# Kernel optimization log

Hardware: AMD Instinct MI355X
Metric: run time of the kernel (lower is better)

## Reference

```python
import jax, jax.numpy as jnp
import numpy as np

NV, NE, H, P = 50000, 10000, 256, 400000

def setup_inputs() -> dict:
    key = jax.random.key(0)
    ks = jax.random.split(key, 16)
    s = 1.0 / np.sqrt(H)
    return {
        "v": jax.random.normal(ks[0], (NV, H), jnp.float32),
        "e": jax.random.normal(ks[1], (NE, H), jnp.float32),
        "W_v2e_w": jax.random.normal(ks[2], (H, H), jnp.float32) * s,
        "W_v2e_b": jnp.zeros((H,), jnp.float32),
        "W_e2v_w": jax.random.normal(ks[3], (H, H), jnp.float32) * s,
        "W_e2v_b": jnp.zeros((H,), jnp.float32),
        "n_weight": jax.random.uniform(ks[4], (NV, 1), jnp.float32),
        "e_weight": jax.random.uniform(ks[5], (NE, 1), jnp.float32),
        "n_reg_weight": jax.random.uniform(ks[6], (P, 1), jnp.float32),
        "e_reg_weight": jax.random.uniform(ks[7], (P, 1), jnp.float32),
        "e_reg_sum": jax.random.uniform(ks[8], (NE, 1), jnp.float32) + 1.0,  # positive normalizer
        "n_reg_sum": jax.random.uniform(ks[9], (NV, 1), jnp.float32) + 1.0,
        "pairs_v": jax.random.randint(ks[10], (P,), 0, NV, jnp.int32),  # ve_lists[:,0]
        "eidx": jax.random.randint(ks[11], (P,), 0, NE, jnp.int32),
        "pairs_e": jax.random.randint(ks[12], (P,), 0, NE, jnp.int32),  # ve_lists[:,1]
        "vidx": jax.random.randint(ks[13], (P,), 0, NV, jnp.int32),
    }

def reference(v, e, W_v2e_w, W_v2e_b, W_e2v_w, W_e2v_b, n_weight, e_weight,
              n_reg_weight, e_reg_weight, e_reg_sum, n_reg_sum,
              pairs_v, eidx, pairs_e, vidx):
    # v2e: dense transform on vertices, gather per incidence, scatter-add into edges
    ve = jax.nn.relu(v @ W_v2e_w.T + W_v2e_b)            # [NV,H]
    v_acc = v * n_weight                                 # v *= n_weight * v_fac(=1)
    msg_ve = (ve * n_weight)[pairs_v] * n_reg_weight     # [P,H]
    e_out = e.at[eidx].add(msg_ve) / e_reg_sum           # [NE,H]
    # e2v: dense transform on edges, gather per incidence, scatter-add into vertices
    ev = jax.nn.relu(e_out @ W_e2v_w.T + W_e2v_b)        # [NE,H]
    msg_ev = (ev * e_weight)[pairs_e] * e_reg_weight     # [P,H]
    v_out = v_acc.at[vidx].add(msg_ev) / n_reg_sum       # [NV,H]
    return v_out, e_out
```

## Files before the change

kernel.cpp:

```cpp
#include <hip/hip_runtime.h>
#include <stdint.h>

#define NV 50000
#define NE 10000
#define HD 256
#define NP 400000

#define SE 88
#define SV 36

#define NCH 128
#define CHP (NP / NCH)
#define NW  15000
#define NWE 2500
#define NWV 12500

#define PREP_HBLK NCH
#define PREP_WBLK 16
#define PREP_VBLK 1563

typedef short short8 __attribute__((ext_vector_type(8)));
typedef short short4v __attribute__((ext_vector_type(4)));
typedef float f32x4 __attribute__((ext_vector_type(4)));

__device__ __forceinline__ short f2bf(float f) {
    unsigned int u = __builtin_bit_cast(unsigned int, f);
    u += 0x7FFFu + ((u >> 16) & 1u);
    return (short)(u >> 16);
}
__device__ __forceinline__ float bf2f(short s) {
    unsigned int u = ((unsigned int)(unsigned short)s) << 16;
    return __builtin_bit_cast(float, u);
}

__global__ __launch_bounds__(1024) void prep_kernel(
    const float* __restrict__ v, const float* __restrict__ W1, const float* __restrict__ W2,
    const int* __restrict__ eidx, const int* __restrict__ vidx,
    short* __restrict__ v_bf, short* __restrict__ W_bf,
    int* __restrict__ cnt8,
    int conv_v)
{
    __shared__ int h[NW];
    int b = blockIdx.x;
    int tid = threadIdx.x;
    if (b < PREP_HBLK) {
        for (int w = tid; w < NW; w += 1024) h[w] = 0;
        __syncthreads();
        int base = b * CHP;
        for (int k = tid; k < CHP; k += 1024) {
            int p = base + k;
            int er = eidx[p];
            atomicAdd((unsigned*)&h[er >> 2], 1u << ((er & 3) * 8));
            int rv = 10000 + vidx[p];
            atomicAdd((unsigned*)&h[rv >> 2], 1u << ((rv & 3) * 8));
        }
        __syncthreads();
        for (int w = tid; w < NW; w += 1024) cnt8[b * NW + w] = h[w];
    } else if (b < PREP_HBLK + PREP_WBLK) {
        size_t i = (size_t)(b - PREP_HBLK) * 8192 + (size_t)tid * 8;
        const float* src = (i < 65536) ? (W1 + i) : (W2 + (i - 65536));
        float4 a0 = *(const float4*)src;
        float4 a1 = *(const float4*)(src + 4);
        short8 s;
        s[0] = f2bf(a0.x); s[1] = f2bf(a0.y); s[2] = f2bf(a0.z); s[3] = f2bf(a0.w);
        s[4] = f2bf(a1.x); s[5] = f2bf(a1.y); s[6] = f2bf(a1.z); s[7] = f2bf(a1.w);
        *(short8*)(W_bf + i) = s;
    } else {
        if (!conv_v) return;
        size_t i = (size_t)(b - PREP_HBLK - PREP_WBLK) * 8192 + (size_t)tid * 8;
        if (i >= (size_t)NV * HD) return;
        float4 a0 = *(const float4*)(v + i);
        float4 a1 = *(const float4*)(v + i + 4);
        short8 s;
        s[0] = f2bf(a0.x); s[1] = f2bf(a0.y); s[2] = f2bf(a0.z); s[3] = f2bf(a0.w);
        s[4] = f2bf(a1.x); s[5] = f2bf(a1.y); s[6] = f2bf(a1.z); s[7] = f2bf(a1.w);
        *(short8*)(v_bf + i) = s;
    }
}

__global__ __launch_bounds__(256) void scan_kernel(
    int* __restrict__ cnt8, int* __restrict__ cnt_e, int* __restrict__ cnt_v)
{
    int w = blockIdx.x * 256 + threadIdx.x;
    if (w >= NW) return;
    unsigned acc = 0;
#pragma unroll 8
    for (int c = 0; c < NCH; ++c) {
        unsigned x = (unsigned)cnt8[c * NW + w];
        cnt8[c * NW + w] = (int)acc;
        acc += x;
    }
    int r0 = w * 4;
    int4 t;
    t.x = acc & 0xFF; t.y = (acc >> 8) & 0xFF; t.z = (acc >> 16) & 0xFF; t.w = acc >> 24;
    if (r0 < 10000) *(int4*)&cnt_e[r0] = t;
    else            *(int4*)&cnt_v[r0 - 10000] = t;
}

__global__ __launch_bounds__(1024) void place_kernel(
    const int* __restrict__ eidx, const int* __restrict__ vidx,
    const int* __restrict__ pairs_v, const int* __restrict__ n_reg_w_bits,
    const int* __restrict__ pairs_e, const int* __restrict__ e_reg_w_bits,
    const int* __restrict__ cnt8,
    int2* __restrict__ bkt_e, int2* __restrict__ bkt_v)
{
    __shared__ int h[NWV];
    int b = blockIdx.x;
    int tid = threadIdx.x;
    if (b < NCH) {
        int c = b;
        for (int w = tid; w < NWE; w += 1024) h[w] = cnt8[c * NW + w];
        __syncthreads();
        int base = c * CHP;
        for (int k = tid; k < CHP; k += 1024) {
            int p = base + k;
            int er = eidx[p];
            unsigned old = atomicAdd((unsigned*)&h[er >> 2], 1u << ((er & 3) * 8));
            int s = (old >> ((er & 3) * 8)) & 0xFF;
            if (s < SE) bkt_e[er * SE + s] = make_int2(pairs_v[p], n_reg_w_bits[p]);
        }
    } else {
        int c = b - NCH;
        for (int w = tid; w < NWV; w += 1024) h[w] = cnt8[c * NW + NWE + w];
        __syncthreads();
        int base = c * CHP;
        for (int k = tid; k < CHP; k += 1024) {
            int p = base + k;
            int vr = vidx[p];
            unsigned old = atomicAdd((unsigned*)&h[vr >> 2], 1u << ((vr & 3) * 8));
            int s = (old >> ((vr & 3) * 8)) & 0xFF;
            if (s < SV) bkt_v[vr * SV + s] = make_int2(pairs_e[p], e_reg_w_bits[p]);
        }
    }
}

__global__ __launch_bounds__(256) void gemm_rs(
    const void* __restrict__ Av, int a_bf,
    const short* __restrict__ Wb,
    const float* __restrict__ bias,
    const float* __restrict__ rowscale,
    short* __restrict__ out,
    int M)
{
    __shared__ short As[64 * 256];
    __shared__ short Ws[64 * 256];
    const int tid  = threadIdx.x;
    const int row0 = blockIdx.x * 64;

#pragma unroll
    for (int it = 0; it < 8; ++it) {
        int cl = it * 256 + tid;
        int r  = cl >> 5;
        int c  = cl & 31;
        int gr = row0 + r; gr = gr < M ? gr : M - 1;
        short8 ap;
        if (a_bf) {
            ap = *(const short8*)((const short*)Av + (size_t)gr * HD + (c << 3));
        } else {
            const float* asrc = (const float*)Av + (size_t)gr * HD + (c << 3);
            float4 a0 = *(const float4*)asrc;
            float4 a1 = *(const float4*)(asrc + 4);
            ap[0] = f2bf(a0.x); ap[1] = f2bf(a0.y); ap[2] = f2bf(a0.z); ap[3] = f2bf(a0.w);
            ap[4] = f2bf(a1.x); ap[5] = f2bf(a1.y); ap[6] = f2bf(a1.z); ap[7] = f2bf(a1.w);
        }
        *(short8*)&As[(r << 8) + ((c ^ (r & 7)) << 3)] = ap;
    }

    const int lane = tid & 63;
    const int wv   = tid >> 6;
    const int m16  = lane & 15;
    const int quad = lane >> 4;
    const int arow = (wv << 4) + m16;

    for (int ct = 0; ct < 4; ++ct) {
        __syncthreads();
#pragma unroll
        for (int it = 0; it < 8; ++it) {
            int cl = it * 256 + tid;
            int r  = cl >> 5;
            int c  = cl & 31;
            short8 wp = *(const short8*)(Wb + (size_t)((ct << 6) + r) * HD + (c << 3));
            *(short8*)&Ws[(r << 8) + ((c ^ (r & 7)) << 3)] = wp;
        }
        __syncthreads();

        f32x4 acc[4];
#pragma unroll
        for (int nt = 0; nt < 4; ++nt) acc[nt] = (f32x4){0.f, 0.f, 0.f, 0.f};

#pragma unroll
        for (int ks = 0; ks < 8; ++ks) {
            int c = (ks << 2) + quad;
            short8 afr = *(const short8*)&As[(arow << 8) + ((c ^ (arow & 7)) << 3)];
#pragma unroll
            for (int nt = 0; nt < 4; ++nt) {
                int brow = (nt << 4) + m16;
                short8 bfr = *(const short8*)&Ws[(brow << 8) + ((c ^ (m16 & 7)) << 3)];
                acc[nt] = __builtin_amdgcn_mfma_f32_16x16x32_bf16(afr, bfr, acc[nt], 0, 0, 0);
            }
        }

#pragma unroll
        for (int r = 0; r < 4; ++r) {
            int row = row0 + (wv << 4) + (quad << 2) + r;
            if (row < M) {
                float rs = rowscale[row];
#pragma unroll
                for (int nt = 0; nt < 4; ++nt) {
                    int col = (ct << 6) + (nt << 4) + m16;
                    float val = acc[nt][r] + bias[col];
                    val = fmaxf(val, 0.0f) * rs;
                    out[(size_t)row * HD + col] = f2bf(val);
                }
            }
        }
    }
}

__device__ __forceinline__ void gather_core(
    const short* __restrict__ msg, const int2* __restrict__ bkt,
    int i, int end, int lane, float4& acc)
{
    while (i < end) {
        int n = end - i; n = n < 64 ? n : 64;
        int src = 0; float w = 0.f;
        if (lane < n) {
            int2 m = bkt[i + lane];
            src = m.x;
            w = __builtin_bit_cast(float, m.y);
        }
        int j = 0;
        for (; j + 4 <= n; j += 4) {
            int   s0 = __shfl(src, j),     s1 = __shfl(src, j + 1);
            int   s2 = __shfl(src, j + 2), s3 = __shfl(src, j + 3);
            float w0 = __shfl(w, j),       w1 = __shfl(w, j + 1);
            float w2 = __shfl(w, j + 2),   w3 = __shfl(w, j + 3);
            short4v m0 = *(const short4v*)(msg + ((size_t)s0 << 8) + (lane << 2));
            short4v m1 = *(const short4v*)(msg + ((size_t)s1 << 8) + (lane << 2));
            short4v m2 = *(const short4v*)(msg + ((size_t)s2 << 8) + (lane << 2));
            short4v m3 = *(const short4v*)(msg + ((size_t)s3 << 8) + (lane << 2));
            acc.x += bf2f(m0[0]) * w0; acc.y += bf2f(m0[1]) * w0;
            acc.z += bf2f(m0[2]) * w0; acc.w += bf2f(m0[3]) * w0;
            acc.x += bf2f(m1[0]) * w1; acc.y += bf2f(m1[1]) * w1;
            acc.z += bf2f(m1[2]) * w1; acc.w += bf2f(m1[3]) * w1;
            acc.x += bf2f(m2[0]) * w2; acc.y += bf2f(m2[1]) * w2;
            acc.z += bf2f(m2[2]) * w2; acc.w += bf2f(m2[3]) * w2;
            acc.x += bf2f(m3[0]) * w3; acc.y += bf2f(m3[1]) * w3;
            acc.z += bf2f(m3[2]) * w3; acc.w += bf2f(m3[3]) * w3;
        }
        for (; j < n; ++j) {
            int s0 = __shfl(src, j); float w0 = __shfl(w, j);
            short4v m0 = *(const short4v*)(msg + ((size_t)s0 << 8) + (lane << 2));
            acc.x += bf2f(m0[0]) * w0; acc.y += bf2f(m0[1]) * w0;
            acc.z += bf2f(m0[2]) * w0; acc.w += bf2f(m0[3]) * w0;
        }
        i += n;
    }
}

__global__ __launch_bounds__(256) void gather_e(
    const short* __restrict__ msg,
    const int2* __restrict__ bkt,
    const int* __restrict__ cnt,
    const float* __restrict__ e_in, const float* __restrict__ reg_sum,
    float* __restrict__ out, short* __restrict__ out_bf)
{
    int r    = (blockIdx.x << 2) + (threadIdx.x >> 6);
    int lane = threadIdx.x & 63;
    float4 acc = ((const float4*)(e_in + (size_t)r * HD))[lane];
    int n = cnt[r]; n = n < SE ? n : SE;
    int i0 = r * SE;
    gather_core(msg, bkt, i0, i0 + n, lane, acc);
    float inv = 1.0f / reg_sum[r];
    acc.x *= inv; acc.y *= inv; acc.z *= inv; acc.w *= inv;
    ((float4*)(out + (size_t)r * HD))[lane] = acc;
    if (out_bf) {
        short4v s;
        s[0] = f2bf(acc.x); s[1] = f2bf(acc.y); s[2] = f2bf(acc.z); s[3] = f2bf(acc.w);
        *(short4v*)(out_bf + (size_t)r * HD + (lane << 2)) = s;
    }
}

__global__ __launch_bounds__(256) void gather_v(
    const short* __restrict__ msg,
    const int2* __restrict__ bkt,
    const int* __restrict__ cnt,
    const float* __restrict__ v_f32, const short* __restrict__ v_bf,
    const float* __restrict__ n_w,
    const float* __restrict__ reg_sum, float* __restrict__ out)
{
    int r    = (blockIdx.x << 2) + (threadIdx.x >> 6);
    int lane = threadIdx.x & 63;
    float nw = n_w[r];
    float4 a;
    if (v_bf) {
        short4v b = *(const short4v*)(v_bf + (size_t)r * HD + (lane << 2));
        a.x = bf2f(b[0]); a.y = bf2f(b[1]); a.z = bf2f(b[2]); a.w = bf2f(b[3]);
    } else {
        a = ((const float4*)(v_f32 + (size_t)r * HD))[lane];
    }
    float4 acc; acc.x = a.x * nw; acc.y = a.y * nw; acc.z = a.z * nw; acc.w = a.w * nw;
    int n = cnt[r]; n = n < SV ? n : SV;
    int i0 = r * SV;
    gather_core(msg, bkt, i0, i0 + n, lane, acc);
    float inv = 1.0f / reg_sum[r];
    acc.x *= inv; acc.y *= inv; acc.z *= inv; acc.w *= inv;
    ((float4*)(out + (size_t)r * HD))[lane] = acc;
}

extern "C" void kernel_launch(void* const* d_in, const int* in_sizes, int n_in,
                              void* d_out, int out_size, void* d_ws, size_t ws_size,
                              hipStream_t stream) {
    const float* v   = (const float*)d_in[0];
    const float* e   = (const float*)d_in[1];
    const float* W1  = (const float*)d_in[2];
    const float* b1  = (const float*)d_in[3];
    const float* W2  = (const float*)d_in[4];
    const float* b2  = (const float*)d_in[5];
    const float* n_weight     = (const float*)d_in[6];
    const float* e_weight     = (const float*)d_in[7];
    const float* n_reg_weight = (const float*)d_in[8];
    const float* e_reg_weight = (const float*)d_in[9];
    const float* e_reg_sum    = (const float*)d_in[10];
    const float* n_reg_sum    = (const float*)d_in[11];
    const int* pairs_v = (const int*)d_in[12];
    const int* eidx    = (const int*)d_in[13];
    const int* pairs_e = (const int*)d_in[14];
    const int* vidx    = (const int*)d_in[15];

    float* out      = (float*)d_out;
    float* v_region = out;
    float* e_region = out + (size_t)NV * HD;

    char* ws = (char*)d_ws;
    size_t o = 0;
    short* msg     = (short*)(ws + o); o += (size_t)NV * HD * 2;
    int2*  bkt_e   = (int2*)(ws + o);  o += (size_t)NE * SE * 8;
    int2*  bkt_v   = (int2*)(ws + o);  o += (size_t)NV * SV * 8;
    short* W_bf    = (short*)(ws + o); o += (size_t)2 * 65536 * 2;
    int*   cnt8    = (int*)(ws + o);
    short* e_bf    = (short*)(ws + o); o += (size_t)NCH * NW * 4;
    int*   cnt_e   = (int*)(ws + o);   o += (size_t)NE * 4;
    int*   cnt_v   = (int*)(ws + o);   o += (size_t)NV * 4;
    size_t o_opt = o;
    short* v_bf    = (short*)(ws + o_opt);
    size_t need_full = o_opt + (size_t)NV * HD * 2;
    const int full = (ws_size >= need_full);

    prep_kernel<<<PREP_HBLK + PREP_WBLK + PREP_VBLK, 1024, 0, stream>>>(
        v, W1, W2, eidx, vidx, full ? v_bf : (short*)msg , W_bf,
        cnt8, full);
    scan_kernel<<<(NW + 255) / 256, 256, 0, stream>>>(cnt8, cnt_e, cnt_v);
    place_kernel<<<2 * NCH, 1024, 0, stream>>>(
        eidx, vidx, pairs_v, (const int*)n_reg_weight,
        pairs_e, (const int*)e_reg_weight, cnt8, bkt_e, bkt_v);

    gemm_rs<<<(NV + 63) / 64, 256, 0, stream>>>(
        full ? (const void*)v_bf : (const void*)v, full, W_bf, b1, n_weight, msg, NV);
    gather_e<<<NE / 4, 256, 0, stream>>>(msg, bkt_e, cnt_e,
        e, e_reg_sum, e_region, e_bf);
    gemm_rs<<<(NE + 63) / 64, 256, 0, stream>>>(
        (const void*)e_bf, 1, W_bf + 65536, b2, e_weight, msg, NE);
    gather_v<<<NV / 4, 256, 0, stream>>>(msg, bkt_v, cnt_v,
        v, full ? v_bf : (short*)0, n_weight, n_reg_sum, v_region);
}
```

Measured before the change: 275.1 us.

## Fuse v bf16 conversion into GEMM and restructure gather with preloaded buckets

The standalone fp32-to-bf16 conversion of v in the prep kernel is removed. The first GEMM now reads fp32 v directly, converts it while staging into shared memory, and writes the bf16 copy out for the later gather_v pass, which saves one full read of v. The gather routine is rewritten: each wave loads its bucket window once up front with a single load, the inner loop is unrolled to 8, and two accumulators break the add dependency chain. Bucket buffers are padded by 64 entries so the unconditional 64-lane window load stays in bounds.

```diff
diff --git a/kernel.cpp b/kernel.cpp
--- a/kernel.cpp
+++ b/kernel.cpp
@@ -17,7 +17,6 @@
 
 #define PREP_HBLK NCH
 #define PREP_WBLK 16
-#define PREP_VBLK 1563
 
 typedef short short8 __attribute__((ext_vector_type(8)));
 typedef short short4v __attribute__((ext_vector_type(4)));
@@ -34,11 +33,10 @@
 }
 
 __global__ __launch_bounds__(1024) void prep_kernel(
-    const float* __restrict__ v, const float* __restrict__ W1, const float* __restrict__ W2,
+    const float* __restrict__ W1, const float* __restrict__ W2,
     const int* __restrict__ eidx, const int* __restrict__ vidx,
-    short* __restrict__ v_bf, short* __restrict__ W_bf,
-    int* __restrict__ cnt8,
-    int conv_v)
+    short* __restrict__ W_bf,
+    int* __restrict__ cnt8)
 {
     __shared__ int h[NW];
     int b = blockIdx.x;
@@ -56,7 +54,7 @@
         }
         __syncthreads();
         for (int w = tid; w < NW; w += 1024) cnt8[b * NW + w] = h[w];
-    } else if (b < PREP_HBLK + PREP_WBLK) {
+    } else {
         size_t i = (size_t)(b - PREP_HBLK) * 8192 + (size_t)tid * 8;
         const float* src = (i < 65536) ? (W1 + i) : (W2 + (i - 65536));
         float4 a0 = *(const float4*)src;
@@ -65,16 +63,6 @@
         s[0] = f2bf(a0.x); s[1] = f2bf(a0.y); s[2] = f2bf(a0.z); s[3] = f2bf(a0.w);
         s[4] = f2bf(a1.x); s[5] = f2bf(a1.y); s[6] = f2bf(a1.z); s[7] = f2bf(a1.w);
         *(short8*)(W_bf + i) = s;
-    } else {
-        if (!conv_v) return;
-        size_t i = (size_t)(b - PREP_HBLK - PREP_WBLK) * 8192 + (size_t)tid * 8;
-        if (i >= (size_t)NV * HD) return;
-        float4 a0 = *(const float4*)(v + i);
-        float4 a1 = *(const float4*)(v + i + 4);
-        short8 s;
-        s[0] = f2bf(a0.x); s[1] = f2bf(a0.y); s[2] = f2bf(a0.z); s[3] = f2bf(a0.w);
-        s[4] = f2bf(a1.x); s[5] = f2bf(a1.y); s[6] = f2bf(a1.z); s[7] = f2bf(a1.w);
-        *(short8*)(v_bf + i) = s;
     }
 }
 
@@ -140,6 +128,7 @@
     const float* __restrict__ bias,
     const float* __restrict__ rowscale,
     short* __restrict__ out,
+    short* __restrict__ a_out,
     int M)
 {
     __shared__ short As[64 * 256];
@@ -152,7 +141,8 @@
         int cl = it * 256 + tid;
         int r  = cl >> 5;
         int c  = cl & 31;
-        int gr = row0 + r; gr = gr < M ? gr : M - 1;
+        int gr0 = row0 + r;
+        int gr  = gr0 < M ? gr0 : M - 1;
         short8 ap;
         if (a_bf) {
             ap = *(const short8*)((const short*)Av + (size_t)gr * HD + (c << 3));
@@ -162,6 +152,8 @@
             float4 a1 = *(const float4*)(asrc + 4);
             ap[0] = f2bf(a0.x); ap[1] = f2bf(a0.y); ap[2] = f2bf(a0.z); ap[3] = f2bf(a0.w);
             ap[4] = f2bf(a1.x); ap[5] = f2bf(a1.y); ap[6] = f2bf(a1.z); ap[7] = f2bf(a1.w);
+            if (a_out && gr0 < M)
+                *(short8*)(a_out + (size_t)gr0 * HD + (c << 3)) = ap;
         }
         *(short8*)&As[(r << 8) + ((c ^ (r & 7)) << 3)] = ap;
     }
@@ -217,44 +209,66 @@
     }
 }
 
-__device__ __forceinline__ void gather_core(
-    const short* __restrict__ msg, const int2* __restrict__ bkt,
-    int i, int end, int lane, float4& acc)
-{
-    while (i < end) {
-        int n = end - i; n = n < 64 ? n : 64;
-        int src = 0; float w = 0.f;
-        if (lane < n) {
-            int2 m = bkt[i + lane];
-            src = m.x;
-            w = __builtin_bit_cast(float, m.y);
-        }
-        int j = 0;
-        for (; j + 4 <= n; j += 4) {
-            int   s0 = __shfl(src, j),     s1 = __shfl(src, j + 1);
-            int   s2 = __shfl(src, j + 2), s3 = __shfl(src, j + 3);
-            float w0 = __shfl(w, j),       w1 = __shfl(w, j + 1);
-            float w2 = __shfl(w, j + 2),   w3 = __shfl(w, j + 3);
-            short4v m0 = *(const short4v*)(msg + ((size_t)s0 << 8) + (lane << 2));
-            short4v m1 = *(const short4v*)(msg + ((size_t)s1 << 8) + (lane << 2));
-            short4v m2 = *(const short4v*)(msg + ((size_t)s2 << 8) + (lane << 2));
-            short4v m3 = *(const short4v*)(msg + ((size_t)s3 << 8) + (lane << 2));
-            acc.x += bf2f(m0[0]) * w0; acc.y += bf2f(m0[1]) * w0;
-            acc.z += bf2f(m0[2]) * w0; acc.w += bf2f(m0[3]) * w0;
-            acc.x += bf2f(m1[0]) * w1; acc.y += bf2f(m1[1]) * w1;
-            acc.z += bf2f(m1[2]) * w1; acc.w += bf2f(m1[3]) * w1;
-            acc.x += bf2f(m2[0]) * w2; acc.y += bf2f(m2[1]) * w2;
-            acc.z += bf2f(m2[2]) * w2; acc.w += bf2f(m2[3]) * w2;
-            acc.x += bf2f(m3[0]) * w3; acc.y += bf2f(m3[1]) * w3;
-            acc.z += bf2f(m3[2]) * w3; acc.w += bf2f(m3[3]) * w3;
-        }
-        for (; j < n; ++j) {
-            int s0 = __shfl(src, j); float w0 = __shfl(w, j);
-            short4v m0 = *(const short4v*)(msg + ((size_t)s0 << 8) + (lane << 2));
-            acc.x += bf2f(m0[0]) * w0; acc.y += bf2f(m0[1]) * w0;
-            acc.z += bf2f(m0[2]) * w0; acc.w += bf2f(m0[3]) * w0;
-        }
-        i += n;
+__device__ __forceinline__ void gather_win(
+    const short* __restrict__ msg, int src, int wb, int cnt, int lane,
+    float4& A, float4& B)
+{
+    int j = 0;
+    for (; j + 8 <= cnt; j += 8) {
+        int s0 = __shfl(src, j),     s1 = __shfl(src, j + 1);
+        int s2 = __shfl(src, j + 2), s3 = __shfl(src, j + 3);
+        int s4 = __shfl(src, j + 4), s5 = __shfl(src, j + 5);
+        int s6 = __shfl(src, j + 6), s7 = __shfl(src, j + 7);
+        float w0 = __builtin_bit_cast(float, __shfl(wb, j));
+        float w1 = __builtin_bit_cast(float, __shfl(wb, j + 1));
+        float w2 = __builtin_bit_cast(float, __shfl(wb, j + 2));
+        float w3 = __builtin_bit_cast(float, __shfl(wb, j + 3));
+        float w4 = __builtin_bit_cast(float, __shfl(wb, j + 4));
+        float w5 = __builtin_bit_cast(float, __shfl(wb, j + 5));
+        float w6 = __builtin_bit_cast(float, __shfl(wb, j + 6));
+        float w7 = __builtin_bit_cast(float, __shfl(wb, j + 7));
+        short4v m0 = *(const short4v*)(msg + ((size_t)s0 << 8) + (lane << 2));
+        short4v m1 = *(const short4v*)(msg + ((size_t)s1 << 8) + (lane << 2));
+        short4v m2 = *(const short4v*)(msg + ((size_t)s2 << 8) + (lane << 2));
+        short4v m3 = *(const short4v*)(msg + ((size_t)s3 << 8) + (lane << 2));
+        short4v m4 = *(const short4v*)(msg + ((size_t)s4 << 8) + (lane << 2));
+        short4v m5 = *(const short4v*)(msg + ((size_t)s5 << 8) + (lane << 2));
+        short4v m6 = *(const short4v*)(msg + ((size_t)s6 << 8) + (lane << 2));
+        short4v m7 = *(const short4v*)(msg + ((size_t)s7 << 8) + (lane << 2));
+        A.x += bf2f(m0[0]) * w0; A.y += bf2f(m0[1]) * w0;
+        A.z += bf2f(m0[2]) * w0; A.w += bf2f(m0[3]) * w0;
+        B.x += bf2f(m1[0]) * w1; B.y += bf2f(m1[1]) * w1;
+        B.z += bf2f(m1[2]) * w1; B.w += bf2f(m1[3]) * w1;
+        A.x += bf2f(m2[0]) * w2; A.y += bf2f(m2[1]) * w2;
+        A.z += bf2f(m2[2]) * w2; A.w += bf2f(m2[3]) * w2;
+        B.x += bf2f(m3[0]) * w3; B.y += bf2f(m3[1]) * w3;
+        B.z += bf2f(m3[2]) * w3; B.w += bf2f(m3[3]) * w3;
+        A.x += bf2f(m4[0]) * w4; A.y += bf2f(m4[1]) * w4;
+        A.z += bf2f(m4[2]) * w4; A.w += bf2f(m4[3]) * w4;
+        B.x += bf2f(m5[0]) * w5; B.y += bf2f(m5[1]) * w5;
+        B.z += bf2f(m5[2]) * w5; B.w += bf2f(m5[3]) * w5;
+        A.x += bf2f(m6[0]) * w6; A.y += bf2f(m6[1]) * w6;
+        A.z += bf2f(m6[2]) * w6; A.w += bf2f(m6[3]) * w6;
+        B.x += bf2f(m7[0]) * w7; B.y += bf2f(m7[1]) * w7;
+        B.z += bf2f(m7[2]) * w7; B.w += bf2f(m7[3]) * w7;
+    }
+    for (; j + 2 <= cnt; j += 2) {
+        int s0 = __shfl(src, j), s1 = __shfl(src, j + 1);
+        float w0 = __builtin_bit_cast(float, __shfl(wb, j));
+        float w1 = __builtin_bit_cast(float, __shfl(wb, j + 1));
+        short4v m0 = *(const short4v*)(msg + ((size_t)s0 << 8) + (lane << 2));
+        short4v m1 = *(const short4v*)(msg + ((size_t)s1 << 8) + (lane << 2));
+        A.x += bf2f(m0[0]) * w0; A.y += bf2f(m0[1]) * w0;
+        A.z += bf2f(m0[2]) * w0; A.w += bf2f(m0[3]) * w0;
+        B.x += bf2f(m1[0]) * w1; B.y += bf2f(m1[1]) * w1;
+        B.z += bf2f(m1[2]) * w1; B.w += bf2f(m1[3]) * w1;
+    }
+    if (j < cnt) {
+        int s0 = __shfl(src, j);
+        float w0 = __builtin_bit_cast(float, __shfl(wb, j));
+        short4v m0 = *(const short4v*)(msg + ((size_t)s0 << 8) + (lane << 2));
+        A.x += bf2f(m0[0]) * w0; A.y += bf2f(m0[1]) * w0;
+        A.z += bf2f(m0[2]) * w0; A.w += bf2f(m0[3]) * w0;
     }
 }
 
@@ -267,12 +281,22 @@
 {
     int r    = (blockIdx.x << 2) + (threadIdx.x >> 6);
     int lane = threadIdx.x & 63;
-    float4 acc = ((const float4*)(e_in + (size_t)r * HD))[lane];
+    int i0 = r * SE;
+    int2 q = bkt[i0 + lane];
     int n = cnt[r]; n = n < SE ? n : SE;
-    int i0 = r * SE;
-    gather_core(msg, bkt, i0, i0 + n, lane, acc);
+    float4 A = ((const float4*)(e_in + (size_t)r * HD))[lane];
+    float4 B = {0.f, 0.f, 0.f, 0.f};
     float inv = 1.0f / reg_sum[r];
-    acc.x *= inv; acc.y *= inv; acc.z *= inv; acc.w *= inv;
+    int n0 = n < 64 ? n : 64;
+    gather_win(msg, q.x, q.y, n0, lane, A, B);
+    if (n > 64) {
+        int2 q2 = make_int2(0, 0);
+        if (lane < SE - 64) q2 = bkt[i0 + 64 + lane];
+        gather_win(msg, q2.x, q2.y, n - 64, lane, A, B);
+    }
+    float4 acc;
+    acc.x = (A.x + B.x) * inv; acc.y = (A.y + B.y) * inv;
+    acc.z = (A.z + B.z) * inv; acc.w = (A.w + B.w) * inv;
     ((float4*)(out + (size_t)r * HD))[lane] = acc;
     if (out_bf) {
         short4v s;
@@ -291,7 +315,11 @@
 {
     int r    = (blockIdx.x << 2) + (threadIdx.x >> 6);
     int lane = threadIdx.x & 63;
+    int i0 = r * SV;
+    int2 q = bkt[i0 + lane];
+    int n = cnt[r]; n = n < SV ? n : SV;
     float nw = n_w[r];
+    float inv = 1.0f / reg_sum[r];
     float4 a;
     if (v_bf) {
         short4v b = *(const short4v*)(v_bf + (size_t)r * HD + (lane << 2));
@@ -299,12 +327,12 @@
     } else {
         a = ((const float4*)(v_f32 + (size_t)r * HD))[lane];
     }
-    float4 acc; acc.x = a.x * nw; acc.y = a.y * nw; acc.z = a.z * nw; acc.w = a.w * nw;
-    int n = cnt[r]; n = n < SV ? n : SV;
-    int i0 = r * SV;
-    gather_core(msg, bkt, i0, i0 + n, lane, acc);
-    float inv = 1.0f / reg_sum[r];
-    acc.x *= inv; acc.y *= inv; acc.z *= inv; acc.w *= inv;
+    float4 A; A.x = a.x * nw; A.y = a.y * nw; A.z = a.z * nw; A.w = a.w * nw;
+    float4 B = {0.f, 0.f, 0.f, 0.f};
+    gather_win(msg, q.x, q.y, n, lane, A, B);
+    float4 acc;
+    acc.x = (A.x + B.x) * inv; acc.y = (A.y + B.y) * inv;
+    acc.z = (A.z + B.z) * inv; acc.w = (A.w + B.w) * inv;
     ((float4*)(out + (size_t)r * HD))[lane] = acc;
 }
 
@@ -335,8 +363,8 @@
     char* ws = (char*)d_ws;
     size_t o = 0;
     short* msg     = (short*)(ws + o); o += (size_t)NV * HD * 2;
-    int2*  bkt_e   = (int2*)(ws + o);  o += (size_t)NE * SE * 8;
-    int2*  bkt_v   = (int2*)(ws + o);  o += (size_t)NV * SV * 8;
+    int2*  bkt_e   = (int2*)(ws + o);  o += ((size_t)NE * SE + 64) * 8;
+    int2*  bkt_v   = (int2*)(ws + o);  o += ((size_t)NV * SV + 64) * 8;
     short* W_bf    = (short*)(ws + o); o += (size_t)2 * 65536 * 2;
     int*   cnt8    = (int*)(ws + o);
     short* e_bf    = (short*)(ws + o); o += (size_t)NCH * NW * 4;
@@ -347,20 +375,19 @@
     size_t need_full = o_opt + (size_t)NV * HD * 2;
     const int full = (ws_size >= need_full);
 
-    prep_kernel<<<PREP_HBLK + PREP_WBLK + PREP_VBLK, 1024, 0, stream>>>(
-        v, W1, W2, eidx, vidx, full ? v_bf : (short*)msg , W_bf,
-        cnt8, full);
+    prep_kernel<<<PREP_HBLK + PREP_WBLK, 1024, 0, stream>>>(
+        W1, W2, eidx, vidx, W_bf, cnt8);
     scan_kernel<<<(NW + 255) / 256, 256, 0, stream>>>(cnt8, cnt_e, cnt_v);
     place_kernel<<<2 * NCH, 1024, 0, stream>>>(
         eidx, vidx, pairs_v, (const int*)n_reg_weight,
         pairs_e, (const int*)e_reg_weight, cnt8, bkt_e, bkt_v);
 
     gemm_rs<<<(NV + 63) / 64, 256, 0, stream>>>(
-        full ? (const void*)v_bf : (const void*)v, full, W_bf, b1, n_weight, msg, NV);
+        (const void*)v, 0, W_bf, b1, n_weight, msg, full ? v_bf : (short*)0, NV);
     gather_e<<<NE / 4, 256, 0, stream>>>(msg, bkt_e, cnt_e,
         e, e_reg_sum, e_region, e_bf);
     gemm_rs<<<(NE + 63) / 64, 256, 0, stream>>>(
-        (const void*)e_bf, 1, W_bf + 65536, b2, e_weight, msg, NE);
+        (const void*)e_bf, 1, W_bf + 65536, b2, e_weight, msg, (short*)0, NE);
     gather_v<<<NV / 4, 256, 0, stream>>>(msg, bkt_v, cnt_v,
         v, full ? v_bf : (short*)0, n_weight, n_reg_sum, v_region);
 }
```

Result: slower. 282.5 us (+2.7%).
